# Kernel optimization log

Hardware: AMD Instinct MI355X
Metric: run time of the kernel (lower is better)

Reference implementation:

```python
import jax, jax.numpy as jnp
import numpy as np

N, F_IN, H, C, E = 100000, 128, 64, 40, 1600000
NEG_SLOPE = 0.2


def setup_inputs() -> dict:
    key = jax.random.key(0)
    ks = jax.random.split(key, 12)
    s = 0.1
    return {
        "x": jax.random.normal(ks[0], (N, F_IN), jnp.float32),
        "edge_index": jax.random.randint(ks[1], (2, E), 0, N, jnp.int32),
        "W1": jax.random.normal(ks[2], (F_IN, H), jnp.float32) * s,
        "a_src1": jax.random.normal(ks[3], (H,), jnp.float32) * s,
        "a_dst1": jax.random.normal(ks[4], (H,), jnp.float32) * s,
        "b1": jnp.zeros((H,), jnp.float32),
        "W2": jax.random.normal(ks[5], (H, H), jnp.float32) * s,
        "a_src2": jax.random.normal(ks[6], (H,), jnp.float32) * s,
        "a_dst2": jax.random.normal(ks[7], (H,), jnp.float32) * s,
        "b2": jnp.zeros((H,), jnp.float32),
        "Wl": jax.random.normal(ks[8], (H, C), jnp.float32) * s,
        "bl": jnp.zeros((C,), jnp.float32),
    }


def gat_conv(x, src, dst, W, a_src, a_dst, b):
    # PyG GATConv, heads=1, self-loops already appended to (src, dst)
    h = x @ W                                   # [N, H]
    alpha_s = h @ a_src                         # [N]
    alpha_d = h @ a_dst                         # [N]
    e = jax.nn.leaky_relu(alpha_s[src] + alpha_d[dst], NEG_SLOPE)  # [E]
    # segment softmax over incoming edges of each target node
    m = jax.ops.segment_max(e, dst, num_segments=x.shape[0])
    ex = jnp.exp(e - m[dst])
    denom = jax.ops.segment_sum(ex, dst, num_segments=x.shape[0])
    w = ex / (denom[dst] + 1e-16)               # [E]
    out = jax.ops.segment_sum(h[src] * w[:, None], dst, num_segments=x.shape[0])
    return out + b


def reference(x, edge_index, W1, a_src1, a_dst1, b1, W2, a_src2, a_dst2, b2, Wl, bl):
    n = x.shape[0]
    loops = jnp.arange(n, dtype=edge_index.dtype)
    src = jnp.concatenate([edge_index[0], loops])
    dst = jnp.concatenate([edge_index[1], loops])
    h = gat_conv(x, src, dst, W1, a_src1, a_dst1, b1)
    h = jax.nn.relu(h)  # dropout p=0 -> identity
    h = gat_conv(h, src, dst, W2, a_src2, a_dst2, b2)
    logits = h @ Wl + bl
    return jax.nn.log_softmax(logits, axis=-1)
```

## Files before the change

kernel.cpp:

```cpp
#include <hip/hip_runtime.h>
#include <math.h>


#define NEG_SLOPE 0.2f
#define NEG_BIG -3.0e38f

#define BSHIFT 9
#define BSIZE 512
#define CEPB 8192
#define ECAP 112
#define CBPAD 256

typedef __bf16 bf16x8 __attribute__((ext_vector_type(8)));
typedef __bf16 bf16x4 __attribute__((ext_vector_type(4)));
typedef float f32x4 __attribute__((ext_vector_type(4)));

__device__ __forceinline__ float lrelu(float x) {
    return x >= 0.f ? x : NEG_SLOPE * x;
}

__device__ __forceinline__ int wave_incl_scan(int v, int lane) {
#pragma unroll
    for (int d = 1; d < 64; d <<= 1) {
        int t = __shfl_up(v, d, 64);
        if (lane >= d) v += t;
    }
    return v;
}


__global__ __launch_bounds__(256) void fused_hist_gemm(
        const int* __restrict__ src, const int* __restrict__ dst,
        int* __restrict__ bucketCount, int* __restrict__ blockHist,
        unsigned* __restrict__ ebuf, int E, int CB,
        const float* __restrict__ X, const float* __restrict__ W,
        const float* __restrict__ a_src, const float* __restrict__ a_dst,
        __bf16* __restrict__ Hout, float* __restrict__ as_, float* __restrict__ ad_,
        int N, int nTiles) {
    constexpr int K = 128;
    __shared__ __bf16 Whi[64][K + 8];
    __shared__ __bf16 Wlo[64][K + 8];
    __shared__ int hist[256];

    if (blockIdx.x < (unsigned)CB) {
        const int t = threadIdx.x;
        hist[t] = 0;
        __syncthreads();
        const int c = blockIdx.x;
        const int e0 = c * CEPB;
        const int e1 = min(e0 + CEPB, E);
        int rr[CEPB / 256];
#pragma unroll
        for (int i = 0; i < CEPB / 256; ++i) {
            int e = e0 + i * 256 + t;
            if (e < e1) rr[i] = atomicAdd(&hist[dst[e] >> BSHIFT], 1);
        }
        __syncthreads();
        int hv = hist[t];
        blockHist[t * CBPAD + c] = hv;
        if (hv > 0) atomicAdd(&bucketCount[t], hv);
#pragma unroll
        for (int i = 0; i < CEPB / 256; ++i) {
            int e = e0 + i * 256 + t;
            if (e < e1) {
                int d = dst[e];
                int b = d >> BSHIFT;
                ebuf[((size_t)b * CB + c) * ECAP + rr[i]] =
                    ((unsigned)src[e] << BSHIFT) | (unsigned)(d & (BSIZE - 1));
            }
        }
        return;
    }

    const int gbid = blockIdx.x - CB;
    for (int idx = threadIdx.x; idx < K * 64; idx += 256) {
        int k = idx >> 6, n = idx & 63;
        float w = W[idx];
        __bf16 hi = (__bf16)w;
        Whi[n][k] = hi;
        Wlo[n][k] = (__bf16)(w - (float)hi);
    }
    __syncthreads();

    const int lane  = threadIdx.x & 63;
    const int wave  = threadIdx.x >> 6;
    const int row16 = lane & 15;
    const int quad  = lane >> 4;

    float asv[4], adv[4];
#pragma unroll
    for (int t = 0; t < 4; ++t) {
        asv[t] = a_src[t * 16 + row16];
        adv[t] = a_dst[t * 16 + row16];
    }

    for (int tile = gbid; tile < nTiles; tile += 1024) {
        const int nbase = tile * 64;
        int gn = nbase + wave * 16 + row16;
        if (gn >= N) gn = N - 1;
        const float* __restrict__ xp = X + (size_t)gn * K + quad * 8;

        float4 xv[K / 16];
#pragma unroll
        for (int c = 0; c < K / 32; ++c) {
            xv[2 * c]     = *(const float4*)(xp + c * 32);
            xv[2 * c + 1] = *(const float4*)(xp + c * 32 + 4);
        }

        f32x4 acc[4] = {{0.f, 0.f, 0.f, 0.f}, {0.f, 0.f, 0.f, 0.f},
                        {0.f, 0.f, 0.f, 0.f}, {0.f, 0.f, 0.f, 0.f}};
#pragma unroll
        for (int kc = 0; kc < K; kc += 32) {
            float xs[8];
            *(float4*)&xs[0] = xv[kc / 16];
            *(float4*)&xs[4] = xv[kc / 16 + 1];
            bf16x8 ahi, alo;
#pragma unroll
            for (int j = 0; j < 8; ++j) {
                __bf16 hi = (__bf16)xs[j];
                ahi[j] = hi;
                alo[j] = (__bf16)(xs[j] - (float)hi);
            }
#pragma unroll
            for (int t = 0; t < 4; ++t) {
                bf16x8 bhi = *(const bf16x8*)&Whi[t * 16 + row16][kc + quad * 8];
                bf16x8 blo = *(const bf16x8*)&Wlo[t * 16 + row16][kc + quad * 8];
                acc[t] = __builtin_amdgcn_mfma_f32_16x16x32_bf16(ahi, bhi, acc[t], 0, 0, 0);
                acc[t] = __builtin_amdgcn_mfma_f32_16x16x32_bf16(ahi, blo, acc[t], 0, 0, 0);
                acc[t] = __builtin_amdgcn_mfma_f32_16x16x32_bf16(alo, bhi, acc[t], 0, 0, 0);
            }
        }

        float ps[4] = {0.f, 0.f, 0.f, 0.f};
        float pd[4] = {0.f, 0.f, 0.f, 0.f};
#pragma unroll
        for (int t = 0; t < 4; ++t) {
#pragma unroll
            for (int r = 0; r < 4; ++r) {
                int gm = nbase + wave * 16 + quad * 4 + r;
                if (gm < N) Hout[(size_t)gm * 64 + t * 16 + row16] = (__bf16)acc[t][r];
                ps[r] = fmaf(acc[t][r], asv[t], ps[r]);
                pd[r] = fmaf(acc[t][r], adv[t], pd[r]);
            }
        }
#pragma unroll
        for (int r = 0; r < 4; ++r) {
#pragma unroll
            for (int d = 1; d < 16; d <<= 1) {
                ps[r] += __shfl_xor(ps[r], d, 64);
                pd[r] += __shfl_xor(pd[r], d, 64);
            }
        }
        if (row16 == 0) {
#pragma unroll
            for (int r = 0; r < 4; ++r) {
                int gm = nbase + wave * 16 + quad * 4 + r;
                if (gm < N) { as_[gm] = ps[r]; ad_[gm] = pd[r]; }
            }
        }
    }
}


__global__ __launch_bounds__(1024) void bucket_fill(const unsigned* __restrict__ ebuf,
                                                    const int* __restrict__ blockHist,
                                                    const int* __restrict__ bucketCount,
                                                    int* __restrict__ offs,
                                                    int* __restrict__ csr,
                                                    int N, int E, int CB) {
    __shared__ int hist[512], excls[512], bhist_s[256], wsum[16], gsum[16];
    const int b = blockIdx.x;
    const int t = threadIdx.x;
    const int lane = t & 63;
    const int w = t >> 6;

    int v = (t < 256 && t < b) ? bucketCount[t] : 0;
#pragma unroll
    for (int d = 32; d; d >>= 1) v += __shfl_xor(v, d, 64);
    if (lane == 0) gsum[w] = v;
    if (t < 512) hist[t] = 0;
    if (t < 256) bhist_s[t] = blockHist[b * CBPAD + t];
    if (b == 0 && t == 0) offs[N] = E;
    __syncthreads();
    int gbase = 0;
#pragma unroll
    for (int i = 0; i < 16; ++i) gbase += gsum[i];

    int rr[32];
#pragma unroll
    for (int ci = 0; ci < 16; ++ci) {
        int c = w + ci * 16;
        int cnt = (c < CB) ? bhist_s[c] : 0;
        const unsigned* __restrict__ ep = ebuf + ((size_t)b * CB + c) * ECAP;
#pragma unroll
        for (int ri = 0; ri < 2; ++ri) {
            int idx = ri * 64 + lane;
            if (idx < cnt) {
                unsigned rec = ep[idx];
                rr[ci * 2 + ri] = atomicAdd(&hist[rec & (BSIZE - 1)], 1);
            }
        }
    }
    __syncthreads();

    int hv = (t < 512) ? hist[t] : 0;
    int incl = wave_incl_scan(hv, lane);
    if (lane == 63 && w < 8) wsum[w] = incl;
    __syncthreads();
    if (t < 512) {
        int pre = 0;
#pragma unroll
        for (int i = 0; i < 8; ++i) pre += (i < w) ? wsum[i] : 0;
        int excl = incl - hv + pre;
        int n = b * BSIZE + t;
        if (n < N) offs[n] = gbase + excl;
        excls[t] = excl;
    }
    __syncthreads();

#pragma unroll
    for (int ci = 0; ci < 16; ++ci) {
        int c = w + ci * 16;
        int cnt = (c < CB) ? bhist_s[c] : 0;
        const unsigned* __restrict__ ep = ebuf + ((size_t)b * CB + c) * ECAP;
#pragma unroll
        for (int ri = 0; ri < 2; ++ri) {
            int idx = ri * 64 + lane;
            if (idx < cnt) {
                unsigned rec = ep[idx];
                csr[gbase + excls[rec & (BSIZE - 1)] + rr[ci * 2 + ri]] =
                    (int)(rec >> BSHIFT);
            }
        }
    }
}


__global__ __launch_bounds__(256) void gemm_mfma2(const __bf16* __restrict__ X,
                                                  const float* __restrict__ W,
                                                  const float* __restrict__ a_src,
                                                  const float* __restrict__ a_dst,
                                                  __bf16* __restrict__ Hout,
                                                  float* __restrict__ as_,
                                                  float* __restrict__ ad_,
                                                  int N, int nTiles) {
    constexpr int K = 64;
    __shared__ __bf16 Whi[64][K + 8];
    __shared__ __bf16 Wlo[64][K + 8];
    for (int idx = threadIdx.x; idx < K * 64; idx += 256) {
        int k = idx >> 6, n = idx & 63;
        float w = W[idx];
        __bf16 hi = (__bf16)w;
        Whi[n][k] = hi;
        Wlo[n][k] = (__bf16)(w - (float)hi);
    }
    __syncthreads();

    const int lane  = threadIdx.x & 63;
    const int wave  = threadIdx.x >> 6;
    const int row16 = lane & 15;
    const int quad  = lane >> 4;

    float asv[4], adv[4];
#pragma unroll
    for (int t = 0; t < 4; ++t) {
        asv[t] = a_src[t * 16 + row16];
        adv[t] = a_dst[t * 16 + row16];
    }

    for (int tile = blockIdx.x; tile < nTiles; tile += gridDim.x) {
        const int nbase = tile * 64;
        int gn = nbase + wave * 16 + row16;
        if (gn >= N) gn = N - 1;
        const __bf16* __restrict__ xp = X + (size_t)gn * K + quad * 8;
        bf16x8 a0 = *(const bf16x8*)(xp);
        bf16x8 a1 = *(const bf16x8*)(xp + 32);

        f32x4 acc[4] = {{0.f, 0.f, 0.f, 0.f}, {0.f, 0.f, 0.f, 0.f},
                        {0.f, 0.f, 0.f, 0.f}, {0.f, 0.f, 0.f, 0.f}};
#pragma unroll
        for (int kc = 0; kc < K; kc += 32) {
            bf16x8 a = (kc == 0) ? a0 : a1;
#pragma unroll
            for (int t = 0; t < 4; ++t) {
                bf16x8 bhi = *(const bf16x8*)&Whi[t * 16 + row16][kc + quad * 8];
                bf16x8 blo = *(const bf16x8*)&Wlo[t * 16 + row16][kc + quad * 8];
                acc[t] = __builtin_amdgcn_mfma_f32_16x16x32_bf16(a, bhi, acc[t], 0, 0, 0);
                acc[t] = __builtin_amdgcn_mfma_f32_16x16x32_bf16(a, blo, acc[t], 0, 0, 0);
            }
        }

        float ps[4] = {0.f, 0.f, 0.f, 0.f};
        float pd[4] = {0.f, 0.f, 0.f, 0.f};
#pragma unroll
        for (int t = 0; t < 4; ++t) {
#pragma unroll
            for (int r = 0; r < 4; ++r) {
                int gm = nbase + wave * 16 + quad * 4 + r;
                if (gm < N) Hout[(size_t)gm * 64 + t * 16 + row16] = (__bf16)acc[t][r];
                ps[r] = fmaf(acc[t][r], asv[t], ps[r]);
                pd[r] = fmaf(acc[t][r], adv[t], pd[r]);
            }
        }
#pragma unroll
        for (int r = 0; r < 4; ++r) {
#pragma unroll
            for (int d = 1; d < 16; d <<= 1) {
                ps[r] += __shfl_xor(ps[r], d, 64);
                pd[r] += __shfl_xor(pd[r], d, 64);
            }
        }
        if (row16 == 0) {
#pragma unroll
            for (int r = 0; r < 4; ++r) {
                int gm = nbase + wave * 16 + quad * 4 + r;
                if (gm < N) { as_[gm] = ps[r]; ad_[gm] = pd[r]; }
            }
        }
    }
}


__global__ __launch_bounds__(256) void gat_agg(const __bf16* __restrict__ h,
                                               const float* __restrict__ as_,
                                               const float* __restrict__ ad_,
                                               const float* __restrict__ bias,
                                               const int* __restrict__ offs,
                                               const int* __restrict__ csr,
                                               __bf16* __restrict__ out,
                                               int N, int do_relu) {
    int gtid = blockIdx.x * blockDim.x + threadIdx.x;
    int n = __builtin_amdgcn_readfirstlane(gtid >> 6);
    if (n >= N) return;
    const int lane = threadIdx.x & 63;
    const int g  = lane >> 4;
    const int fl = lane & 15;

    int beg = offs[n], end = offs[n + 1];
    float adn = ad_[n];
    float p_self = __expf(lrelu(as_[n] + adn));

    float den = p_self;
    float ax, ay, az, aw;
    {
        bf16x4 t = *(const bf16x4*)(h + (size_t)n * 64 + fl * 4);
        float m0 = (g == 0) ? p_self : 0.f;
        ax = m0 * (float)t[0];
        ay = m0 * (float)t[1];
        az = m0 * (float)t[2];
        aw = m0 * (float)t[3];
    }

    for (int c0 = beg; c0 < end; c0 += 64) {
        int cnt = end - c0;
        if (cnt > 64) cnt = 64;
        int   s_l = (lane < cnt) ? csr[c0 + lane] : 0;
        float p_l = (lane < cnt) ? __expf(lrelu(as_[s_l] + adn)) : 0.f;
        float csum = p_l;
#pragma unroll
        for (int d = 32; d; d >>= 1) csum += __shfl_xor(csum, d, 64);
        den += csum;

        int rounds = (cnt + 3) >> 2;
        for (int r = 0; r < rounds; r += 8) {
            int s[8];
#pragma unroll
            for (int i = 0; i < 8; ++i) s[i] = __shfl(s_l, (r + i) * 4 + g, 64);
            bf16x4 hv[8];
#pragma unroll
            for (int i = 0; i < 8; ++i)
                hv[i] = *(const bf16x4*)(h + (size_t)s[i] * 64 + fl * 4);
            float w[8];
#pragma unroll
            for (int i = 0; i < 8; ++i) w[i] = __shfl(p_l, (r + i) * 4 + g, 64);
#pragma unroll
            for (int i = 0; i < 8; ++i) {
                ax = fmaf(w[i], (float)hv[i][0], ax);
                ay = fmaf(w[i], (float)hv[i][1], ay);
                az = fmaf(w[i], (float)hv[i][2], az);
                aw = fmaf(w[i], (float)hv[i][3], aw);
            }
        }
    }

#pragma unroll
    for (int d = 16; d <= 32; d <<= 1) {
        ax += __shfl_xor(ax, d, 64);
        ay += __shfl_xor(ay, d, 64);
        az += __shfl_xor(az, d, 64);
        aw += __shfl_xor(aw, d, 64);
    }
    if (g == 0) {
        float inv = 1.f / (den + 1e-16f);
        const float4 b4 = *(const float4*)(bias + fl * 4);
        bf16x4 ov;
        float o0 = fmaf(ax, inv, b4.x);
        float o1 = fmaf(ay, inv, b4.y);
        float o2 = fmaf(az, inv, b4.z);
        float o3 = fmaf(aw, inv, b4.w);
        if (do_relu) {
            o0 = fmaxf(o0, 0.f); o1 = fmaxf(o1, 0.f);
            o2 = fmaxf(o2, 0.f); o3 = fmaxf(o3, 0.f);
        }
        ov[0] = (__bf16)o0; ov[1] = (__bf16)o1;
        ov[2] = (__bf16)o2; ov[3] = (__bf16)o3;
        *(bf16x4*)(out + (size_t)n * 64 + fl * 4) = ov;
    }
}


__global__ __launch_bounds__(256) void final_lsm(const __bf16* __restrict__ h,
                                                 const float* __restrict__ Wl,
                                                 const float* __restrict__ bl,
                                                 float* __restrict__ out,
                                                 int N, int nTiles) {
    __shared__ __bf16 Whi[48][72];
    __shared__ __bf16 Wlo[48][72];
    __shared__ float bls[48];
    for (int idx = threadIdx.x; idx < 48 * 64; idx += 256) {
        int c = idx >> 6, k = idx & 63;
        float w = (c < 40) ? Wl[k * 40 + c] : 0.f;
        __bf16 hi = (__bf16)w;
        Whi[c][k] = hi;
        Wlo[c][k] = (__bf16)(w - (float)hi);
    }
    if (threadIdx.x < 48) bls[threadIdx.x] = (threadIdx.x < 40) ? bl[threadIdx.x] : 0.f;
    __syncthreads();

    const int lane  = threadIdx.x & 63;
    const int wave  = threadIdx.x >> 6;
    const int col16 = lane & 15;
    const int quad  = lane >> 4;

    for (int tile = blockIdx.x; tile < nTiles; tile += gridDim.x) {
        const int nbase = tile * 64;
        int gn = nbase + wave * 16 + col16;
        if (gn >= N) gn = N - 1;
        const __bf16* __restrict__ xp = h + (size_t)gn * 64 + quad * 8;
        bf16x8 a0 = *(const bf16x8*)(xp);
        bf16x8 a1 = *(const bf16x8*)(xp + 32);

        f32x4 acc[3] = {{0.f, 0.f, 0.f, 0.f}, {0.f, 0.f, 0.f, 0.f},
                        {0.f, 0.f, 0.f, 0.f}};
#pragma unroll
        for (int kc = 0; kc < 64; kc += 32) {
            bf16x8 a = (kc == 0) ? a0 : a1;
#pragma unroll
            for (int t = 0; t < 3; ++t) {
                bf16x8 bhi = *(const bf16x8*)&Whi[t * 16 + col16][kc + quad * 8];
                bf16x8 blo = *(const bf16x8*)&Wlo[t * 16 + col16][kc + quad * 8];
                acc[t] = __builtin_amdgcn_mfma_f32_16x16x32_bf16(a, bhi, acc[t], 0, 0, 0);
                acc[t] = __builtin_amdgcn_mfma_f32_16x16x32_bf16(a, blo, acc[t], 0, 0, 0);
            }
        }

#pragma unroll
        for (int r = 0; r < 4; ++r) {
            int gm = nbase + wave * 16 + quad * 4 + r;
            float l0 = acc[0][r] + bls[col16];
            float l1 = acc[1][r] + bls[16 + col16];
            float l2 = (col16 < 8) ? (acc[2][r] + bls[32 + col16]) : NEG_BIG;
            float mx = fmaxf(fmaxf(l0, l1), l2);
#pragma unroll
            for (int d = 1; d < 16; d <<= 1) mx = fmaxf(mx, __shfl_xor(mx, d, 64));
            float s = __expf(l0 - mx) + __expf(l1 - mx) +
                      ((col16 < 8) ? __expf(l2 - mx) : 0.f);
#pragma unroll
            for (int d = 1; d < 16; d <<= 1) s += __shfl_xor(s, d, 64);
            float lse = mx + __logf(s);
            if (gm < N) {
                out[(size_t)gm * 40 + col16]      = l0 - lse;
                out[(size_t)gm * 40 + 16 + col16] = l1 - lse;
                if (col16 < 8) out[(size_t)gm * 40 + 32 + col16] = l2 - lse;
            }
        }
    }
}


extern "C" void kernel_launch(void* const* d_in, const int* in_sizes, int n_in,
                              void* d_out, int out_size, void* d_ws, size_t ws_size,
                              hipStream_t stream) {
    const float* x      = (const float*)d_in[0];
    const int*   ei     = (const int*)d_in[1];
    const float* W1     = (const float*)d_in[2];
    const float* a_src1 = (const float*)d_in[3];
    const float* a_dst1 = (const float*)d_in[4];
    const float* b1     = (const float*)d_in[5];
    const float* W2     = (const float*)d_in[6];
    const float* a_src2 = (const float*)d_in[7];
    const float* a_dst2 = (const float*)d_in[8];
    const float* b2     = (const float*)d_in[9];
    const float* Wl     = (const float*)d_in[10];
    const float* bl     = (const float*)d_in[11];

    const int N = in_sizes[0] / 128;
    const int E = in_sizes[1] / 2;
    const int* src = ei;
    const int* dst = ei + E;
    const int nbuck = (N + BSIZE - 1) >> BSHIFT;
    const int CB = (E + CEPB - 1) / CEPB;

    char* p = (char*)d_ws;
    auto alloc = [&](size_t bytes) -> void* {
        void* r = (void*)p;
        p += (bytes + 255) & ~(size_t)255;
        return r;
    };
    int*      offs        = (int*)alloc((size_t)(N + 1) * 4);
    int*      bucketCount = (int*)alloc(256 * 4);
    int*      blockHist   = (int*)alloc(256 * CBPAD * 4);
    unsigned* ebuf        = (unsigned*)alloc((size_t)nbuck * CB * ECAP * 4);
    int*      csr         = (int*)alloc((size_t)E * 4);
    __bf16*   hbf         = (__bf16*)alloc((size_t)N * 64 * 2);
    __bf16*   habg        = (__bf16*)alloc((size_t)N * 64 * 2);
    float*    as_         = (float*)alloc((size_t)N * 4);
    float*    ad_         = (float*)alloc((size_t)N * 4);

    hipMemsetAsync(bucketCount, 0, 256 * 4, stream);

    const int nTiles = (N + 63) / 64;
    int aggBlocks = (N * 64 + 255) / 256;

    fused_hist_gemm<<<CB + 1024, 256, 0, stream>>>(
        src, dst, bucketCount, blockHist, ebuf, E, CB,
        x, W1, a_src1, a_dst1, hbf, as_, ad_, N, nTiles);
    bucket_fill<<<nbuck, 1024, 0, stream>>>(ebuf, blockHist, bucketCount,
                                            offs, csr, N, E, CB);
    gat_agg<<<aggBlocks, 256, 0, stream>>>(hbf, as_, ad_, b1, offs, csr, habg, N, 1);
    gemm_mfma2<<<1024, 256, 0, stream>>>(habg, W2, a_src2, a_dst2, hbf, as_, ad_, N, nTiles);
    gat_agg<<<aggBlocks, 256, 0, stream>>>(hbf, as_, ad_, b2, offs, csr, habg, N, 0);
    final_lsm<<<nTiles, 256, 0, stream>>>(habg, Wl, bl, (float*)d_out, N, nTiles);
}
```

Measured before the change: 278.9 us.

## Fuse GAT aggregation with following dense GEMM via shared-memory row tiles

```diff
diff --git a/kernel.cpp b/kernel.cpp
--- a/kernel.cpp
+++ b/kernel.cpp
@@ -236,187 +236,179 @@
 }
 
 
-__global__ __launch_bounds__(256) void gemm_mfma2(const __bf16* __restrict__ X,
-                                                  const float* __restrict__ W,
-                                                  const float* __restrict__ a_src,
-                                                  const float* __restrict__ a_dst,
-                                                  __bf16* __restrict__ Hout,
-                                                  float* __restrict__ as_,
-                                                  float* __restrict__ ad_,
-                                                  int N, int nTiles) {
-    constexpr int K = 64;
-    __shared__ __bf16 Whi[64][K + 8];
-    __shared__ __bf16 Wlo[64][K + 8];
-    for (int idx = threadIdx.x; idx < K * 64; idx += 256) {
+__global__ __launch_bounds__(256) void agg_gemm2(
+        const __bf16* __restrict__ h, const float* __restrict__ as_,
+        const float* __restrict__ ad_, const float* __restrict__ bias,
+        const int* __restrict__ offs, const int* __restrict__ csr,
+        const float* __restrict__ W, const float* __restrict__ a_src2,
+        const float* __restrict__ a_dst2, __bf16* __restrict__ Hout,
+        float* __restrict__ as2, float* __restrict__ ad2, int N) {
+    __shared__ __bf16 Whi[64][72];
+    __shared__ __bf16 Wlo[64][72];
+    __shared__ __bf16 rows[64][68];
+
+    for (int idx = threadIdx.x; idx < 64 * 64; idx += 256) {
         int k = idx >> 6, n = idx & 63;
         float w = W[idx];
         __bf16 hi = (__bf16)w;
         Whi[n][k] = hi;
         Wlo[n][k] = (__bf16)(w - (float)hi);
     }
+
+    const int lane = threadIdx.x & 63;
+    const int wave = threadIdx.x >> 6;
+    const int g  = lane >> 4;
+    const int fl = lane & 15;
+    const int nbase = blockIdx.x * 64;
+    const float4 b4 = *(const float4*)(bias + fl * 4);
+
+    for (int i = 0; i < 16; ++i) {
+        const int slot = wave * 16 + i;
+        const int n = nbase + slot;
+        if (n >= N) {
+            if (g == 0) {
+                bf16x4 z;
+                z[0] = (__bf16)0.f; z[1] = (__bf16)0.f;
+                z[2] = (__bf16)0.f; z[3] = (__bf16)0.f;
+                *(bf16x4*)&rows[slot][fl * 4] = z;
+            }
+            continue;
+        }
+        int beg = offs[n], end = offs[n + 1];
+        float adn = ad_[n];
+        float p_self = __expf(lrelu(as_[n] + adn));
+
+        float den = p_self;
+        float ax, ay, az, aw;
+        {
+            bf16x4 t = *(const bf16x4*)(h + (size_t)n * 64 + fl * 4);
+            float m0 = (g == 0) ? p_self : 0.f;
+            ax = m0 * (float)t[0];
+            ay = m0 * (float)t[1];
+            az = m0 * (float)t[2];
+            aw = m0 * (float)t[3];
+        }
+
+        for (int c0 = beg; c0 < end; c0 += 64) {
+            int cnt = end - c0;
+            if (cnt > 64) cnt = 64;
+            int   s_l = (lane < cnt) ? csr[c0 + lane] : 0;
+            float p_l = (lane < cnt) ? __expf(lrelu(as_[s_l] + adn)) : 0.f;
+            float csum = p_l;
+#pragma unroll
+            for (int d = 32; d; d >>= 1) csum += __shfl_xor(csum, d, 64);
+            den += csum;
+
+            int rounds = (cnt + 3) >> 2;
+            for (int r = 0; r < rounds; r += 8) {
+                int s[8];
+#pragma unroll
+                for (int j = 0; j < 8; ++j) s[j] = __shfl(s_l, (r + j) * 4 + g, 64);
+                bf16x4 hv[8];
+#pragma unroll
+                for (int j = 0; j < 8; ++j)
+                    hv[j] = *(const bf16x4*)(h + (size_t)s[j] * 64 + fl * 4);
+                float w8[8];
+#pragma unroll
+                for (int j = 0; j < 8; ++j) w8[j] = __shfl(p_l, (r + j) * 4 + g, 64);
+#pragma unroll
+                for (int j = 0; j < 8; ++j) {
+                    ax = fmaf(w8[j], (float)hv[j][0], ax);
+                    ay = fmaf(w8[j], (float)hv[j][1], ay);
+                    az = fmaf(w8[j], (float)hv[j][2], az);
+                    aw = fmaf(w8[j], (float)hv[j][3], aw);
+                }
+            }
+        }
+
+#pragma unroll
+        for (int d = 16; d <= 32; d <<= 1) {
+            ax += __shfl_xor(ax, d, 64);
+            ay += __shfl_xor(ay, d, 64);
+            az += __shfl_xor(az, d, 64);
+            aw += __shfl_xor(aw, d, 64);
+        }
+        if (g == 0) {
+            float inv = 1.f / (den + 1e-16f);
+            bf16x4 ov;
+            ov[0] = (__bf16)fmaxf(fmaf(ax, inv, b4.x), 0.f);
+            ov[1] = (__bf16)fmaxf(fmaf(ay, inv, b4.y), 0.f);
+            ov[2] = (__bf16)fmaxf(fmaf(az, inv, b4.z), 0.f);
+            ov[3] = (__bf16)fmaxf(fmaf(aw, inv, b4.w), 0.f);
+            *(bf16x4*)&rows[slot][fl * 4] = ov;
+        }
+    }
     __syncthreads();
 
-    const int lane  = threadIdx.x & 63;
-    const int wave  = threadIdx.x >> 6;
     const int row16 = lane & 15;
     const int quad  = lane >> 4;
 
     float asv[4], adv[4];
 #pragma unroll
     for (int t = 0; t < 4; ++t) {
-        asv[t] = a_src[t * 16 + row16];
-        adv[t] = a_dst[t * 16 + row16];
-    }
-
-    for (int tile = blockIdx.x; tile < nTiles; tile += gridDim.x) {
-        const int nbase = tile * 64;
-        int gn = nbase + wave * 16 + row16;
-        if (gn >= N) gn = N - 1;
-        const __bf16* __restrict__ xp = X + (size_t)gn * K + quad * 8;
-        bf16x8 a0 = *(const bf16x8*)(xp);
-        bf16x8 a1 = *(const bf16x8*)(xp + 32);
-
-        f32x4 acc[4] = {{0.f, 0.f, 0.f, 0.f}, {0.f, 0.f, 0.f, 0.f},
-                        {0.f, 0.f, 0.f, 0.f}, {0.f, 0.f, 0.f, 0.f}};
-#pragma unroll
-        for (int kc = 0; kc < K; kc += 32) {
-            bf16x8 a = (kc == 0) ? a0 : a1;
-#pragma unroll
-            for (int t = 0; t < 4; ++t) {
-                bf16x8 bhi = *(const bf16x8*)&Whi[t * 16 + row16][kc + quad * 8];
-                bf16x8 blo = *(const bf16x8*)&Wlo[t * 16 + row16][kc + quad * 8];
-                acc[t] = __builtin_amdgcn_mfma_f32_16x16x32_bf16(a, bhi, acc[t], 0, 0, 0);
-                acc[t] = __builtin_amdgcn_mfma_f32_16x16x32_bf16(a, blo, acc[t], 0, 0, 0);
-            }
-        }
-
-        float ps[4] = {0.f, 0.f, 0.f, 0.f};
-        float pd[4] = {0.f, 0.f, 0.f, 0.f};
+        asv[t] = a_src2[t * 16 + row16];
+        adv[t] = a_dst2[t * 16 + row16];
+    }
+
+    const __bf16* xp = &rows[wave * 16 + row16][quad * 8];
+    bf16x8 a0 = *(const bf16x8*)(xp);
+    bf16x8 a1 = *(const bf16x8*)(xp + 32);
+
+    f32x4 acc[4] = {{0.f, 0.f, 0.f, 0.f}, {0.f, 0.f, 0.f, 0.f},
+                    {0.f, 0.f, 0.f, 0.f}, {0.f, 0.f, 0.f, 0.f}};
+#pragma unroll
+    for (int kc = 0; kc < 64; kc += 32) {
+        bf16x8 a = (kc == 0) ? a0 : a1;
 #pragma unroll
         for (int t = 0; t < 4; ++t) {
-#pragma unroll
-            for (int r = 0; r < 4; ++r) {
-                int gm = nbase + wave * 16 + quad * 4 + r;
-                if (gm < N) Hout[(size_t)gm * 64 + t * 16 + row16] = (__bf16)acc[t][r];
-                ps[r] = fmaf(acc[t][r], asv[t], ps[r]);
-                pd[r] = fmaf(acc[t][r], adv[t], pd[r]);
-            }
-        }
+            bf16x8 bhi = *(const bf16x8*)&Whi[t * 16 + row16][kc + quad * 8];
+            bf16x8 blo = *(const bf16x8*)&Wlo[t * 16 + row16][kc + quad * 8];
+            acc[t] = __builtin_amdgcn_mfma_f32_16x16x32_bf16(a, bhi, acc[t], 0, 0, 0);
+            acc[t] = __builtin_amdgcn_mfma_f32_16x16x32_bf16(a, blo, acc[t], 0, 0, 0);
+        }
+    }
+
+    float ps[4] = {0.f, 0.f, 0.f, 0.f};
+    float pd[4] = {0.f, 0.f, 0.f, 0.f};
+#pragma unroll
+    for (int t = 0; t < 4; ++t) {
 #pragma unroll
         for (int r = 0; r < 4; ++r) {
-#pragma unroll
-            for (int d = 1; d < 16; d <<= 1) {
-                ps[r] += __shfl_xor(ps[r], d, 64);
-                pd[r] += __shfl_xor(pd[r], d, 64);
-            }
-        }
-        if (row16 == 0) {
-#pragma unroll
-            for (int r = 0; r < 4; ++r) {
-                int gm = nbase + wave * 16 + quad * 4 + r;
-                if (gm < N) { as_[gm] = ps[r]; ad_[gm] = pd[r]; }
-            }
+            int gm = nbase + wave * 16 + quad * 4 + r;
+            if (gm < N) Hout[(size_t)gm * 64 + t * 16 + row16] = (__bf16)acc[t][r];
+            ps[r] = fmaf(acc[t][r], asv[t], ps[r]);
+            pd[r] = fmaf(acc[t][r], adv[t], pd[r]);
+        }
+    }
+#pragma unroll
+    for (int r = 0; r < 4; ++r) {
+#pragma unroll
+        for (int d = 1; d < 16; d <<= 1) {
+            ps[r] += __shfl_xor(ps[r], d, 64);
+            pd[r] += __shfl_xor(pd[r], d, 64);
+        }
+    }
+    if (row16 == 0) {
+#pragma unroll
+        for (int r = 0; r < 4; ++r) {
+            int gm = nbase + wave * 16 + quad * 4 + r;
+            if (gm < N) { as2[gm] = ps[r]; ad2[gm] = pd[r]; }
         }
     }
 }
 
 
-__global__ __launch_bounds__(256) void gat_agg(const __bf16* __restrict__ h,
-                                               const float* __restrict__ as_,
-                                               const float* __restrict__ ad_,
-                                               const float* __restrict__ bias,
-                                               const int* __restrict__ offs,
-                                               const int* __restrict__ csr,
-                                               __bf16* __restrict__ out,
-                                               int N, int do_relu) {
-    int gtid = blockIdx.x * blockDim.x + threadIdx.x;
-    int n = __builtin_amdgcn_readfirstlane(gtid >> 6);
-    if (n >= N) return;
-    const int lane = threadIdx.x & 63;
-    const int g  = lane >> 4;
-    const int fl = lane & 15;
-
-    int beg = offs[n], end = offs[n + 1];
-    float adn = ad_[n];
-    float p_self = __expf(lrelu(as_[n] + adn));
-
-    float den = p_self;
-    float ax, ay, az, aw;
-    {
-        bf16x4 t = *(const bf16x4*)(h + (size_t)n * 64 + fl * 4);
-        float m0 = (g == 0) ? p_self : 0.f;
-        ax = m0 * (float)t[0];
-        ay = m0 * (float)t[1];
-        az = m0 * (float)t[2];
-        aw = m0 * (float)t[3];
-    }
-
-    for (int c0 = beg; c0 < end; c0 += 64) {
-        int cnt = end - c0;
-        if (cnt > 64) cnt = 64;
-        int   s_l = (lane < cnt) ? csr[c0 + lane] : 0;
-        float p_l = (lane < cnt) ? __expf(lrelu(as_[s_l] + adn)) : 0.f;
-        float csum = p_l;
-#pragma unroll
-        for (int d = 32; d; d >>= 1) csum += __shfl_xor(csum, d, 64);
-        den += csum;
-
-        int rounds = (cnt + 3) >> 2;
-        for (int r = 0; r < rounds; r += 8) {
-            int s[8];
-#pragma unroll
-            for (int i = 0; i < 8; ++i) s[i] = __shfl(s_l, (r + i) * 4 + g, 64);
-            bf16x4 hv[8];
-#pragma unroll
-            for (int i = 0; i < 8; ++i)
-                hv[i] = *(const bf16x4*)(h + (size_t)s[i] * 64 + fl * 4);
-            float w[8];
-#pragma unroll
-            for (int i = 0; i < 8; ++i) w[i] = __shfl(p_l, (r + i) * 4 + g, 64);
-#pragma unroll
-            for (int i = 0; i < 8; ++i) {
-                ax = fmaf(w[i], (float)hv[i][0], ax);
-                ay = fmaf(w[i], (float)hv[i][1], ay);
-                az = fmaf(w[i], (float)hv[i][2], az);
-                aw = fmaf(w[i], (float)hv[i][3], aw);
-            }
-        }
-    }
-
-#pragma unroll
-    for (int d = 16; d <= 32; d <<= 1) {
-        ax += __shfl_xor(ax, d, 64);
-        ay += __shfl_xor(ay, d, 64);
-        az += __shfl_xor(az, d, 64);
-        aw += __shfl_xor(aw, d, 64);
-    }
-    if (g == 0) {
-        float inv = 1.f / (den + 1e-16f);
-        const float4 b4 = *(const float4*)(bias + fl * 4);
-        bf16x4 ov;
-        float o0 = fmaf(ax, inv, b4.x);
-        float o1 = fmaf(ay, inv, b4.y);
-        float o2 = fmaf(az, inv, b4.z);
-        float o3 = fmaf(aw, inv, b4.w);
-        if (do_relu) {
-            o0 = fmaxf(o0, 0.f); o1 = fmaxf(o1, 0.f);
-            o2 = fmaxf(o2, 0.f); o3 = fmaxf(o3, 0.f);
-        }
-        ov[0] = (__bf16)o0; ov[1] = (__bf16)o1;
-        ov[2] = (__bf16)o2; ov[3] = (__bf16)o3;
-        *(bf16x4*)(out + (size_t)n * 64 + fl * 4) = ov;
-    }
-}
-
-
-__global__ __launch_bounds__(256) void final_lsm(const __bf16* __restrict__ h,
-                                                 const float* __restrict__ Wl,
-                                                 const float* __restrict__ bl,
-                                                 float* __restrict__ out,
-                                                 int N, int nTiles) {
+__global__ __launch_bounds__(256) void agg_final(
+        const __bf16* __restrict__ h, const float* __restrict__ as_,
+        const float* __restrict__ ad_, const float* __restrict__ bias,
+        const int* __restrict__ offs, const int* __restrict__ csr,
+        const float* __restrict__ Wl, const float* __restrict__ bl,
+        float* __restrict__ out, int N) {
     __shared__ __bf16 Whi[48][72];
     __shared__ __bf16 Wlo[48][72];
     __shared__ float bls[48];
+    __shared__ __bf16 rows[64][68];
+
     for (int idx = threadIdx.x; idx < 48 * 64; idx += 256) {
         int c = idx >> 6, k = idx & 63;
         float w = (c < 40) ? Wl[k * 40 + c] : 0.f;
@@ -425,54 +417,131 @@
         Wlo[c][k] = (__bf16)(w - (float)hi);
     }
     if (threadIdx.x < 48) bls[threadIdx.x] = (threadIdx.x < 40) ? bl[threadIdx.x] : 0.f;
+
+    const int lane = threadIdx.x & 63;
+    const int wave = threadIdx.x >> 6;
+    const int g  = lane >> 4;
+    const int fl = lane & 15;
+    const int nbase = blockIdx.x * 64;
+    const float4 b4 = *(const float4*)(bias + fl * 4);
+
+    for (int i = 0; i < 16; ++i) {
+        const int slot = wave * 16 + i;
+        const int n = nbase + slot;
+        if (n >= N) {
+            if (g == 0) {
+                bf16x4 z;
+                z[0] = (__bf16)0.f; z[1] = (__bf16)0.f;
+                z[2] = (__bf16)0.f; z[3] = (__bf16)0.f;
+                *(bf16x4*)&rows[slot][fl * 4] = z;
+            }
+            continue;
+        }
+        int beg = offs[n], end = offs[n + 1];
+        float adn = ad_[n];
+        float p_self = __expf(lrelu(as_[n] + adn));
+
+        float den = p_self;
+        float ax, ay, az, aw;
+        {
+            bf16x4 t = *(const bf16x4*)(h + (size_t)n * 64 + fl * 4);
+            float m0 = (g == 0) ? p_self : 0.f;
+            ax = m0 * (float)t[0];
+            ay = m0 * (float)t[1];
+            az = m0 * (float)t[2];
+            aw = m0 * (float)t[3];
+        }
+
+        for (int c0 = beg; c0 < end; c0 += 64) {
+            int cnt = end - c0;
+            if (cnt > 64) cnt = 64;
+            int   s_l = (lane < cnt) ? csr[c0 + lane] : 0;
+            float p_l = (lane < cnt) ? __expf(lrelu(as_[s_l] + adn)) : 0.f;
+            float csum = p_l;
+#pragma unroll
+            for (int d = 32; d; d >>= 1) csum += __shfl_xor(csum, d, 64);
+            den += csum;
+
+            int rounds = (cnt + 3) >> 2;
+            for (int r = 0; r < rounds; r += 8) {
+                int s[8];
+#pragma unroll
+                for (int j = 0; j < 8; ++j) s[j] = __shfl(s_l, (r + j) * 4 + g, 64);
+                bf16x4 hv[8];
+#pragma unroll
+                for (int j = 0; j < 8; ++j)
+                    hv[j] = *(const bf16x4*)(h + (size_t)s[j] * 64 + fl * 4);
+                float w8[8];
+#pragma unroll
+                for (int j = 0; j < 8; ++j) w8[j] = __shfl(p_l, (r + j) * 4 + g, 64);
+#pragma unroll
+                for (int j = 0; j < 8; ++j) {
+                    ax = fmaf(w8[j], (float)hv[j][0], ax);
+                    ay = fmaf(w8[j], (float)hv[j][1], ay);
+                    az = fmaf(w8[j], (float)hv[j][2], az);
+                    aw = fmaf(w8[j], (float)hv[j][3], aw);
+                }
+            }
+        }
+
+#pragma unroll
+        for (int d = 16; d <= 32; d <<= 1) {
+            ax += __shfl_xor(ax, d, 64);
+            ay += __shfl_xor(ay, d, 64);
+            az += __shfl_xor(az, d, 64);
+            aw += __shfl_xor(aw, d, 64);
+        }
+        if (g == 0) {
+            float inv = 1.f / (den + 1e-16f);
+            bf16x4 ov;
+            ov[0] = (__bf16)fmaf(ax, inv, b4.x);
+            ov[1] = (__bf16)fmaf(ay, inv, b4.y);
+            ov[2] = (__bf16)fmaf(az, inv, b4.z);
+            ov[3] = (__bf16)fmaf(aw, inv, b4.w);
+            *(bf16x4*)&rows[slot][fl * 4] = ov;
+        }
+    }
     __syncthreads();
 
-    const int lane  = threadIdx.x & 63;
-    const int wave  = threadIdx.x >> 6;
     const int col16 = lane & 15;
     const int quad  = lane >> 4;
 
-    for (int tile = blockIdx.x; tile < nTiles; tile += gridDim.x) {
-        const int nbase = tile * 64;
-        int gn = nbase + wave * 16 + col16;
-        if (gn >= N) gn = N - 1;
-        const __bf16* __restrict__ xp = h + (size_t)gn * 64 + quad * 8;
-        bf16x8 a0 = *(const bf16x8*)(xp);
-        bf16x8 a1 = *(const bf16x8*)(xp + 32);
-
-        f32x4 acc[3] = {{0.f, 0.f, 0.f, 0.f}, {0.f, 0.f, 0.f, 0.f},
-                        {0.f, 0.f, 0.f, 0.f}};
-#pragma unroll
-        for (int kc = 0; kc < 64; kc += 32) {
-            bf16x8 a = (kc == 0) ? a0 : a1;
-#pragma unroll
-            for (int t = 0; t < 3; ++t) {
-                bf16x8 bhi = *(const bf16x8*)&Whi[t * 16 + col16][kc + quad * 8];
-                bf16x8 blo = *(const bf16x8*)&Wlo[t * 16 + col16][kc + quad * 8];
-                acc[t] = __builtin_amdgcn_mfma_f32_16x16x32_bf16(a, bhi, acc[t], 0, 0, 0);
-                acc[t] = __builtin_amdgcn_mfma_f32_16x16x32_bf16(a, blo, acc[t], 0, 0, 0);
-            }
-        }
-
-#pragma unroll
-        for (int r = 0; r < 4; ++r) {
-            int gm = nbase + wave * 16 + quad * 4 + r;
-            float l0 = acc[0][r] + bls[col16];
-            float l1 = acc[1][r] + bls[16 + col16];
-            float l2 = (col16 < 8) ? (acc[2][r] + bls[32 + col16]) : NEG_BIG;
-            float mx = fmaxf(fmaxf(l0, l1), l2);
-#pragma unroll
-            for (int d = 1; d < 16; d <<= 1) mx = fmaxf(mx, __shfl_xor(mx, d, 64));
-            float s = __expf(l0 - mx) + __expf(l1 - mx) +
-                      ((col16 < 8) ? __expf(l2 - mx) : 0.f);
-#pragma unroll
-            for (int d = 1; d < 16; d <<= 1) s += __shfl_xor(s, d, 64);
-            float lse = mx + __logf(s);
-            if (gm < N) {
-                out[(size_t)gm * 40 + col16]      = l0 - lse;
-                out[(size_t)gm * 40 + 16 + col16] = l1 - lse;
-                if (col16 < 8) out[(size_t)gm * 40 + 32 + col16] = l2 - lse;
-            }
+    const __bf16* xp = &rows[wave * 16 + col16][quad * 8];
+    bf16x8 a0 = *(const bf16x8*)(xp);
+    bf16x8 a1 = *(const bf16x8*)(xp + 32);
+
+    f32x4 acc[3] = {{0.f, 0.f, 0.f, 0.f}, {0.f, 0.f, 0.f, 0.f},
+                    {0.f, 0.f, 0.f, 0.f}};
+#pragma unroll
+    for (int kc = 0; kc < 64; kc += 32) {
+        bf16x8 a = (kc == 0) ? a0 : a1;
+#pragma unroll
+        for (int t = 0; t < 3; ++t) {
+            bf16x8 bhi = *(const bf16x8*)&Whi[t * 16 + col16][kc + quad * 8];
+            bf16x8 blo = *(const bf16x8*)&Wlo[t * 16 + col16][kc + quad * 8];
+            acc[t] = __builtin_amdgcn_mfma_f32_16x16x32_bf16(a, bhi, acc[t], 0, 0, 0);
+            acc[t] = __builtin_amdgcn_mfma_f32_16x16x32_bf16(a, blo, acc[t], 0, 0, 0);
+        }
+    }
+
+#pragma unroll
+    for (int r = 0; r < 4; ++r) {
+        int gm = nbase + wave * 16 + quad * 4 + r;
+        float l0 = acc[0][r] + bls[col16];
+        float l1 = acc[1][r] + bls[16 + col16];
+        float l2 = (col16 < 8) ? (acc[2][r] + bls[32 + col16]) : NEG_BIG;
+        float mx = fmaxf(fmaxf(l0, l1), l2);
+#pragma unroll
+        for (int d = 1; d < 16; d <<= 1) mx = fmaxf(mx, __shfl_xor(mx, d, 64));
+        float s = __expf(l0 - mx) + __expf(l1 - mx) +
+                  ((col16 < 8) ? __expf(l2 - mx) : 0.f);
+#pragma unroll
+        for (int d = 1; d < 16; d <<= 1) s += __shfl_xor(s, d, 64);
+        float lse = mx + __logf(s);
+        if (gm < N) {
+            out[(size_t)gm * 40 + col16]      = l0 - lse;
+            out[(size_t)gm * 40 + 16 + col16] = l1 - lse;
+            if (col16 < 8) out[(size_t)gm * 40 + 32 + col16] = l2 - lse;
         }
     }
 }
@@ -513,22 +582,23 @@
     unsigned* ebuf        = (unsigned*)alloc((size_t)nbuck * CB * ECAP * 4);
     int*      csr         = (int*)alloc((size_t)E * 4);
     __bf16*   hbf         = (__bf16*)alloc((size_t)N * 64 * 2);
-    __bf16*   habg        = (__bf16*)alloc((size_t)N * 64 * 2);
+    __bf16*   hbf2        = (__bf16*)alloc((size_t)N * 64 * 2);
     float*    as_         = (float*)alloc((size_t)N * 4);
     float*    ad_         = (float*)alloc((size_t)N * 4);
+    float*    as2_        = (float*)alloc((size_t)N * 4);
+    float*    ad2_        = (float*)alloc((size_t)N * 4);
 
     hipMemsetAsync(bucketCount, 0, 256 * 4, stream);
 
     const int nTiles = (N + 63) / 64;
-    int aggBlocks = (N * 64 + 255) / 256;
 
     fused_hist_gemm<<<CB + 1024, 256, 0, stream>>>(
         src, dst, bucketCount, blockHist, ebuf, E, CB,
         x, W1, a_src1, a_dst1, hbf, as_, ad_, N, nTiles);
     bucket_fill<<<nbuck, 1024, 0, stream>>>(ebuf, blockHist, bucketCount,
                                             offs, csr, N, E, CB);
-    gat_agg<<<aggBlocks, 256, 0, stream>>>(hbf, as_, ad_, b1, offs, csr, habg, N, 1);
-    gemm_mfma2<<<1024, 256, 0, stream>>>(habg, W2, a_src2, a_dst2, hbf, as_, ad_, N, nTiles);
-    gat_agg<<<aggBlocks, 256, 0, stream>>>(hbf, as_, ad_, b2, offs, csr, habg, N, 0);
-    final_lsm<<<nTiles, 256, 0, stream>>>(habg, Wl, bl, (float*)d_out, N, nTiles);
+    agg_gemm2<<<nTiles, 256, 0, stream>>>(hbf, as_, ad_, b1, offs, csr,
+                                          W2, a_src2, a_dst2, hbf2, as2_, ad2_, N);
+    agg_final<<<nTiles, 256, 0, stream>>>(hbf2, as2_, ad2_, b2, offs, csr,
+                                          Wl, bl, (float*)d_out, N);
 }
```

Result: slower. 334.3 us (+19.9%).

## Reassociate layer-2 GAT to aggregate before W2 and fold W2 into classifier

Applied to the files above, without the earlier changes.

```diff
diff --git a/kernel.cpp b/kernel.cpp
--- a/kernel.cpp
+++ b/kernel.cpp
@@ -36,7 +36,12 @@
         const float* __restrict__ X, const float* __restrict__ W,
         const float* __restrict__ a_src, const float* __restrict__ a_dst,
         __bf16* __restrict__ Hout, float* __restrict__ as_, float* __restrict__ ad_,
-        int N, int nTiles) {
+        int N, int nTiles,
+        const float* __restrict__ W2g, const float* __restrict__ Wlg,
+        const float* __restrict__ blg, const float* __restrict__ b2g,
+        const float* __restrict__ a_src2, const float* __restrict__ a_dst2,
+        float* __restrict__ Wc, float* __restrict__ bc,
+        float* __restrict__ u2, float* __restrict__ v2) {
     constexpr int K = 128;
     __shared__ __bf16 Whi[64][K + 8];
     __shared__ __bf16 Wlo[64][K + 8];
@@ -68,6 +73,32 @@
                 ebuf[((size_t)b * CB + c) * ECAP + rr[i]] =
                     ((unsigned)src[e] << BSHIFT) | (unsigned)(d & (BSIZE - 1));
             }
+        }
+        return;
+    }
+
+    if (blockIdx.x == (unsigned)(CB + 1024)) {
+        const int t = threadIdx.x;
+        for (int idx = t; idx < 64 * 40; idx += 256) {
+            int k = idx / 40, c = idx - k * 40;
+            float s = 0.f;
+            for (int j = 0; j < 64; ++j) s += W2g[k * 64 + j] * Wlg[j * 40 + c];
+            Wc[idx] = s;
+        }
+        if (t < 40) {
+            float s = blg[t];
+            for (int j = 0; j < 64; ++j) s += b2g[j] * Wlg[j * 40 + t];
+            bc[t] = s;
+        }
+        if (t < 64) {
+            float su = 0.f, sv = 0.f;
+            for (int j = 0; j < 64; ++j) {
+                float w = W2g[t * 64 + j];
+                su += w * a_src2[j];
+                sv += w * a_dst2[j];
+            }
+            u2[t] = su;
+            v2[t] = sv;
         }
         return;
     }
@@ -236,91 +267,6 @@
 }
 
 
-__global__ __launch_bounds__(256) void gemm_mfma2(const __bf16* __restrict__ X,
-                                                  const float* __restrict__ W,
-                                                  const float* __restrict__ a_src,
-                                                  const float* __restrict__ a_dst,
-                                                  __bf16* __restrict__ Hout,
-                                                  float* __restrict__ as_,
-                                                  float* __restrict__ ad_,
-                                                  int N, int nTiles) {
-    constexpr int K = 64;
-    __shared__ __bf16 Whi[64][K + 8];
-    __shared__ __bf16 Wlo[64][K + 8];
-    for (int idx = threadIdx.x; idx < K * 64; idx += 256) {
-        int k = idx >> 6, n = idx & 63;
-        float w = W[idx];
-        __bf16 hi = (__bf16)w;
-        Whi[n][k] = hi;
-        Wlo[n][k] = (__bf16)(w - (float)hi);
-    }
-    __syncthreads();
-
-    const int lane  = threadIdx.x & 63;
-    const int wave  = threadIdx.x >> 6;
-    const int row16 = lane & 15;
-    const int quad  = lane >> 4;
-
-    float asv[4], adv[4];
-#pragma unroll
-    for (int t = 0; t < 4; ++t) {
-        asv[t] = a_src[t * 16 + row16];
-        adv[t] = a_dst[t * 16 + row16];
-    }
-
-    for (int tile = blockIdx.x; tile < nTiles; tile += gridDim.x) {
-        const int nbase = tile * 64;
-        int gn = nbase + wave * 16 + row16;
-        if (gn >= N) gn = N - 1;
-        const __bf16* __restrict__ xp = X + (size_t)gn * K + quad * 8;
-        bf16x8 a0 = *(const bf16x8*)(xp);
-        bf16x8 a1 = *(const bf16x8*)(xp + 32);
-
-        f32x4 acc[4] = {{0.f, 0.f, 0.f, 0.f}, {0.f, 0.f, 0.f, 0.f},
-                        {0.f, 0.f, 0.f, 0.f}, {0.f, 0.f, 0.f, 0.f}};
-#pragma unroll
-        for (int kc = 0; kc < K; kc += 32) {
-            bf16x8 a = (kc == 0) ? a0 : a1;
-#pragma unroll
-            for (int t = 0; t < 4; ++t) {
-                bf16x8 bhi = *(const bf16x8*)&Whi[t * 16 + row16][kc + quad * 8];
-                bf16x8 blo = *(const bf16x8*)&Wlo[t * 16 + row16][kc + quad * 8];
-                acc[t] = __builtin_amdgcn_mfma_f32_16x16x32_bf16(a, bhi, acc[t], 0, 0, 0);
-                acc[t] = __builtin_amdgcn_mfma_f32_16x16x32_bf16(a, blo, acc[t], 0, 0, 0);
-            }
-        }
-
-        float ps[4] = {0.f, 0.f, 0.f, 0.f};
-        float pd[4] = {0.f, 0.f, 0.f, 0.f};
-#pragma unroll
-        for (int t = 0; t < 4; ++t) {
-#pragma unroll
-            for (int r = 0; r < 4; ++r) {
-                int gm = nbase + wave * 16 + quad * 4 + r;
-                if (gm < N) Hout[(size_t)gm * 64 + t * 16 + row16] = (__bf16)acc[t][r];
-                ps[r] = fmaf(acc[t][r], asv[t], ps[r]);
-                pd[r] = fmaf(acc[t][r], adv[t], pd[r]);
-            }
-        }
-#pragma unroll
-        for (int r = 0; r < 4; ++r) {
-#pragma unroll
-            for (int d = 1; d < 16; d <<= 1) {
-                ps[r] += __shfl_xor(ps[r], d, 64);
-                pd[r] += __shfl_xor(pd[r], d, 64);
-            }
-        }
-        if (row16 == 0) {
-#pragma unroll
-            for (int r = 0; r < 4; ++r) {
-                int gm = nbase + wave * 16 + quad * 4 + r;
-                if (gm < N) { as_[gm] = ps[r]; ad_[gm] = pd[r]; }
-            }
-        }
-    }
-}
-
-
 __global__ __launch_bounds__(256) void gat_agg(const __bf16* __restrict__ h,
                                                const float* __restrict__ as_,
                                                const float* __restrict__ ad_,
@@ -328,7 +274,11 @@
                                                const int* __restrict__ offs,
                                                const int* __restrict__ csr,
                                                __bf16* __restrict__ out,
-                                               int N, int do_relu) {
+                                               int N, int do_relu,
+                                               const float* __restrict__ u2,
+                                               const float* __restrict__ v2,
+                                               float* __restrict__ as_out,
+                                               float* __restrict__ ad_out) {
     int gtid = blockIdx.x * blockDim.x + threadIdx.x;
     int n = __builtin_amdgcn_readfirstlane(gtid >> 6);
     if (n >= N) return;
@@ -393,7 +343,6 @@
     if (g == 0) {
         float inv = 1.f / (den + 1e-16f);
         const float4 b4 = *(const float4*)(bias + fl * 4);
-        bf16x4 ov;
         float o0 = fmaf(ax, inv, b4.x);
         float o1 = fmaf(ay, inv, b4.y);
         float o2 = fmaf(az, inv, b4.z);
@@ -402,9 +351,23 @@
             o0 = fmaxf(o0, 0.f); o1 = fmaxf(o1, 0.f);
             o2 = fmaxf(o2, 0.f); o3 = fmaxf(o3, 0.f);
         }
+        bf16x4 ov;
         ov[0] = (__bf16)o0; ov[1] = (__bf16)o1;
         ov[2] = (__bf16)o2; ov[3] = (__bf16)o3;
         *(bf16x4*)(out + (size_t)n * 64 + fl * 4) = ov;
+
+        if (u2 != nullptr) {
+            const float4 u4 = *(const float4*)(u2 + fl * 4);
+            const float4 v4 = *(const float4*)(v2 + fl * 4);
+            float pu = o0 * u4.x + o1 * u4.y + o2 * u4.z + o3 * u4.w;
+            float pv = o0 * v4.x + o1 * v4.y + o2 * v4.z + o3 * v4.w;
+#pragma unroll
+            for (int d = 1; d <= 8; d <<= 1) {
+                pu += __shfl_xor(pu, d, 64);
+                pv += __shfl_xor(pv, d, 64);
+            }
+            if (fl == 0) { as_out[n] = pu; ad_out[n] = pv; }
+        }
     }
 }
 
@@ -509,6 +472,7 @@
     };
     int*      offs        = (int*)alloc((size_t)(N + 1) * 4);
     int*      bucketCount = (int*)alloc(256 * 4);
+    float*    zbias       = (float*)alloc(64 * 4);
     int*      blockHist   = (int*)alloc(256 * CBPAD * 4);
     unsigned* ebuf        = (unsigned*)alloc((size_t)nbuck * CB * ECAP * 4);
     int*      csr         = (int*)alloc((size_t)E * 4);
@@ -516,19 +480,27 @@
     __bf16*   habg        = (__bf16*)alloc((size_t)N * 64 * 2);
     float*    as_         = (float*)alloc((size_t)N * 4);
     float*    ad_         = (float*)alloc((size_t)N * 4);
-
-    hipMemsetAsync(bucketCount, 0, 256 * 4, stream);
+    float*    as2_        = (float*)alloc((size_t)N * 4);
+    float*    ad2_        = (float*)alloc((size_t)N * 4);
+    float*    Wc          = (float*)alloc(64 * 40 * 4);
+    float*    bc          = (float*)alloc(40 * 4);
+    float*    u2          = (float*)alloc(64 * 4);
+    float*    v2          = (float*)alloc(64 * 4);
+
+    hipMemsetAsync(bucketCount, 0, 1024 + 256, stream);
 
     const int nTiles = (N + 63) / 64;
     int aggBlocks = (N * 64 + 255) / 256;
 
-    fused_hist_gemm<<<CB + 1024, 256, 0, stream>>>(
+    fused_hist_gemm<<<CB + 1025, 256, 0, stream>>>(
         src, dst, bucketCount, blockHist, ebuf, E, CB,
-        x, W1, a_src1, a_dst1, hbf, as_, ad_, N, nTiles);
+        x, W1, a_src1, a_dst1, hbf, as_, ad_, N, nTiles,
+        W2, Wl, bl, b2, a_src2, a_dst2, Wc, bc, u2, v2);
     bucket_fill<<<nbuck, 1024, 0, stream>>>(ebuf, blockHist, bucketCount,
                                             offs, csr, N, E, CB);
-    gat_agg<<<aggBlocks, 256, 0, stream>>>(hbf, as_, ad_, b1, offs, csr, habg, N, 1);
-    gemm_mfma2<<<1024, 256, 0, stream>>>(habg, W2, a_src2, a_dst2, hbf, as_, ad_, N, nTiles);
-    gat_agg<<<aggBlocks, 256, 0, stream>>>(hbf, as_, ad_, b2, offs, csr, habg, N, 0);
-    final_lsm<<<nTiles, 256, 0, stream>>>(habg, Wl, bl, (float*)d_out, N, nTiles);
-}
+    gat_agg<<<aggBlocks, 256, 0, stream>>>(hbf, as_, ad_, b1, offs, csr, habg,
+                                           N, 1, u2, v2, as2_, ad2_);
+    gat_agg<<<aggBlocks, 256, 0, stream>>>(habg, as2_, ad2_, zbias, offs, csr, hbf,
+                                           N, 0, nullptr, nullptr, nullptr, nullptr);
+    final_lsm<<<nTiles, 256, 0, stream>>>(hbf, Wc, bc, (float*)d_out, N, nTiles);
+}
```

After: 284.4 us. No clear change (+2.0%).
